# Kernel tuning notes

Measured on AMD Instinct MI355X. Metric: run time of the kernel, lower is better.

## Reference

```python
import jax, jax.numpy as jnp
import numpy as np

N, T, LH, HEADS, C, E = 100000, 24, 64, 4, 16, 1600000
NEG_SLOPE = 0.2  # PyG GATConv leaky_relu slope


def setup_inputs() -> dict:
    key = jax.random.key(0)
    ks = jax.random.split(key, 24)
    s = 0.05
    inp = {
        'input_tensor': jax.random.normal(ks[0], (N, T), jnp.float32),
        'edge_index': jax.random.randint(ks[1], (2, E), 0, N, jnp.int32),
        'edge_attr': jax.random.uniform(ks[2], (E, 1), jnp.float32),
        'knn_mask_short': jax.random.randint(ks[3], (E,), 0, 2, jnp.int32).astype(bool),
        # LSTM layer 1 (input_size=1): gate order i,f,g,o
        'W_ih1': jax.random.normal(ks[4], (4 * LH, 1), jnp.float32) * s,
        'W_hh1': jax.random.normal(ks[5], (4 * LH, LH), jnp.float32) * s,
        'b_ih1': jax.random.normal(ks[6], (4 * LH,), jnp.float32) * s,
        'b_hh1': jax.random.normal(ks[7], (4 * LH,), jnp.float32) * s,
        # LSTM layer 2 (input_size=LH)
        'W_ih2': jax.random.normal(ks[8], (4 * LH, LH), jnp.float32) * s,
        'W_hh2': jax.random.normal(ks[9], (4 * LH, LH), jnp.float32) * s,
        'b_ih2': jax.random.normal(ks[10], (4 * LH,), jnp.float32) * s,
        'b_hh2': jax.random.normal(ks[11], (4 * LH,), jnp.float32) * s,
        # GATConv params
        'gat_lin_w': jax.random.normal(ks[12], (HEADS * C, LH), jnp.float32) * s,
        'gat_lin_edge_w': jax.random.normal(ks[13], (HEADS * C, 1), jnp.float32) * s,
        'att_src': jax.random.normal(ks[14], (HEADS, C), jnp.float32) * s,
        'att_dst': jax.random.normal(ks[15], (HEADS, C), jnp.float32) * s,
        'att_edge': jax.random.normal(ks[16], (HEADS, C), jnp.float32) * s,
        'gat_bias': jax.random.normal(ks[17], (HEADS * C,), jnp.float32) * s,
        # final Linear
        'fc_w': jax.random.normal(ks[18], (1, HEADS * C), jnp.float32) * s,
        'fc_b': jax.random.normal(ks[19], (1,), jnp.float32) * s,
    }
    return inp


def _lstm_cell(x, h, c, W_ih, W_hh, b):
    z = x @ W_ih.T + h @ W_hh.T + b  # (N, 4H)
    i, f, g, o = jnp.split(z, 4, axis=-1)
    c = jax.nn.sigmoid(f) * c + jax.nn.sigmoid(i) * jnp.tanh(g)
    h = jax.nn.sigmoid(o) * jnp.tanh(c)
    return h, c


def reference(input_tensor, edge_index, edge_attr, knn_mask_short,
              W_ih1, W_hh1, b_ih1, b_hh1, W_ih2, W_hh2, b_ih2, b_hh2,
              gat_lin_w, gat_lin_edge_w, att_src, att_dst, att_edge, gat_bias,
              fc_w, fc_b):
    n = input_tensor.shape[0]
    # --- 2-layer LSTM over time, fused per-step (only final h2 needed) ---
    xs = input_tensor.T[:, :, None]  # (T, N, 1)
    b1 = b_ih1 + b_hh1
    b2 = b_ih2 + b_hh2
    z = jnp.zeros((n, LH), input_tensor.dtype)

    def step(carry, x_t):
        h1, c1, h2, c2 = carry
        h1, c1 = _lstm_cell(x_t, h1, c1, W_ih1, W_hh1, b1)
        h2, c2 = _lstm_cell(h1, h2, c2, W_ih2, W_hh2, b2)
        return (h1, c1, h2, c2), None

    (h1, c1, h2, c2), _ = jax.lax.scan(step, (z, z, z, z), xs)
    lstm_out = h2  # (N, LH): last time-step output of layer 2

    # --- GATConv (heads concat, edge_dim=1), eval mode (dropout off) ---
    x = (lstm_out @ gat_lin_w.T).reshape(n, HEADS, C)  # (N, H, C)
    a_src = jnp.einsum('nhc,hc->nh', x, att_src)
    a_dst = jnp.einsum('nhc,hc->nh', x, att_dst)
    src, dst = edge_index[0], edge_index[1]
    e = (edge_attr @ gat_lin_edge_w.T).reshape(-1, HEADS, C)  # (E, H, C)
    a_edge = jnp.einsum('ehc,hc->eh', e, att_edge)
    alpha = jax.nn.leaky_relu(a_src[src] + a_dst[dst] + a_edge, NEG_SLOPE)  # (E, H)
    # mask out non-'short' edges (equivalent to slicing them away)
    alpha = jnp.where(knn_mask_short[:, None], alpha, -1e30)
    amax = jax.ops.segment_max(alpha, dst, num_segments=n)  # (N, H)
    ex = jnp.exp(alpha - amax[dst]) * knn_mask_short[:, None].astype(alpha.dtype)
    denom = jax.ops.segment_sum(ex, dst, num_segments=n)  # (N, H)
    w = ex / jnp.maximum(denom[dst], 1e-16)  # (E, H) attention weights
    msg = x[src] * w[:, :, None]  # (E, H, C)
    out = jax.ops.segment_sum(msg, dst, num_segments=n).reshape(n, HEADS * C) + gat_bias

    out = jax.nn.elu(out)
    y = out @ fc_w.T + fc_b  # (N, 1)
    return y.reshape(n)
```

## Files before the change

### kernel.cpp

```cpp
#include <hip/hip_runtime.h>
#include <hip/hip_bf16.h>

#define T_STEPS 24
#define NSLOPE 0.2f
#define PITCH2 136
#define LOG2E 1.4426950408889634f

typedef _Float16 half8 __attribute__((ext_vector_type(8)));
typedef _Float16 half2_t __attribute__((ext_vector_type(2)));
typedef float floatx4 __attribute__((ext_vector_type(4)));

#if __has_builtin(__builtin_amdgcn_exp2f)
#define EXP2(x) __builtin_amdgcn_exp2f(x)
#else
#define EXP2(x) exp2f(x)
#endif
#define RCP(x) __builtin_amdgcn_rcpf(x)

#define ACT(A0,A1,A2,A3,CS,HP) {                                        \
    float u_ = EXP2(-(A0));                                             \
    float fw = EXP2(-(A1));                                             \
    float v_ = EXP2(-(A2));                                             \
    float xo = EXP2(-(A3));                                             \
    float f_ = RCP(1.f + fw);                                           \
    float ig = (1.f - v_) * RCP((1.f + u_) * (1.f + v_));               \
    float cs = fmaf(f_, (CS), ig * (2.f*LOG2E));                        \
    (CS) = cs;                                                          \
    float z_ = EXP2(-cs);                                               \
    (HP) = (_Float16)((1.f - z_) * RCP((1.f + xo) * (1.f + z_)));       \
}

#define MFMA16(A,B,C) __builtin_amdgcn_mfma_f32_16x16x32_f16((A),(B),(C),0,0,0)

__global__ __launch_bounds__(256) void prep_kernel(
    const float* __restrict__ W_ih1, const float* __restrict__ W_hh1,
    const float* __restrict__ b_ih1, const float* __restrict__ b_hh1,
    const float* __restrict__ W_ih2, const float* __restrict__ W_hh2,
    const float* __restrict__ b_ih2, const float* __restrict__ b_hh2,
    const float* __restrict__ glw, const float* __restrict__ glew,
    const float* __restrict__ atte, const unsigned char* __restrict__ mask_bytes,
    _Float16* __restrict__ W1F, _Float16* __restrict__ W2F, _Float16* __restrict__ W3F,
    float* __restrict__ b2P, float* __restrict__ ke, int* __restrict__ flag,
    int* __restrict__ deg, int nn)
{
    int tid = blockIdx.x*blockDim.x + threadIdx.x;
    int nth = gridDim.x*blockDim.x;
    for (int i = tid; i < nn; i += nth) deg[i] = 0;
    for (int idx = tid; idx < 24576; idx += nth){
        int b = idx & 7;
        int lane = (idx >> 3) & 63;
        int t2 = idx >> 9;
        int kt = t2 % 3;
        int t3 = t2 / 3;
        int m = t3 & 1, w = t3 >> 1;
        int row16 = lane & 15;
        int g = row16 & 3, cl = row16 >> 2;
        int row = g*64 + 8*w + 2*cl + m;
        float sc = (g == 2) ? 2.f*LOG2E : LOG2E;
        int k = (lane>>4)*8 + b;
        float val;
        if (kt < 2){ val = W_hh1[row*64 + 32*kt + k]; }
        else { val = (k == 0) ? W_ih1[row] : (k == 1) ? (b_ih1[row]+b_hh1[row]) : 0.f; }
        W1F[idx] = (_Float16)(val * sc);
    }
    for (int idx = tid; idx < 32768; idx += nth){
        int b = idx & 7;
        int lane = (idx >> 3) & 63;
        int kt = (idx >> 9) & 3;
        int t3 = idx >> 11;
        int m = t3 & 1, w = t3 >> 1;
        int row16 = lane & 15;
        int g = row16 & 3, cl = row16 >> 2;
        int row = g*64 + 8*w + 2*cl + m;
        float sc = (g == 2) ? 2.f*LOG2E : LOG2E;
        int k = 32*kt + (lane>>4)*8 + b;
        W2F[idx] = (_Float16)(((k < 64) ? W_ih2[row*64 + k] : W_hh2[row*64 + (k-64)]) * sc);
    }
    for (int idx = tid; idx < 4096; idx += nth){
        int b = idx & 7, t1 = idx >> 3; int lane = t1 & 63, t2 = t1 >> 6;
        int kt = t2 & 1, w = t2 >> 1;
        int row = 16*w + (lane & 15);
        W3F[idx] = (_Float16)glw[row*64 + 32*kt + (lane>>4)*8 + b];
    }
    for (int idx = tid; idx < 4096; idx += nth){
        int r = idx & 3;
        int lane = (idx >> 2) & 63;
        int m = (idx >> 8) & 1;
        int w = idx >> 9;
        int grp = lane >> 4;
        int row = r*64 + 8*w + 2*grp + m;
        float sc = (r == 2) ? 2.f*LOG2E : LOG2E;
        b2P[idx] = (b_ih2[row] + b_hh2[row]) * sc;
    }
    if (tid < 4){ float s = 0.f; for (int c = 0; c < 16; c++) s += atte[tid*16+c]*glew[tid*16+c]; ke[tid] = s; }
    if (tid == 0){ int nz = 0;
        for (int i = 0; i < 4096; i++){ if ((i&3) != 0 && mask_bytes[i] != 0) nz++; }
        *flag = (nz == 0) ? 1 : 0; }
}

__global__ __launch_bounds__(256) void count_kernel(
    const int* __restrict__ ei, const void* __restrict__ maskp, const int* __restrict__ flag,
    int* __restrict__ deg, int E)
{
    int e = blockIdx.x*256 + threadIdx.x;
    if (e >= E) return;
    bool m = (*flag) ? (((const int*)maskp)[e] != 0) : (((const unsigned char*)maskp)[e] != 0);
    if (!m) return;
    atomicAdd(deg + ei[E + e], 1);
}

__global__ __launch_bounds__(1024) void scan_kernel(
    const int* __restrict__ deg, int* __restrict__ offs, int* __restrict__ cursor, int nn)
{
    __shared__ int wsum[16];
    __shared__ int sbase;
    int lane = threadIdx.x & 63, wv = threadIdx.x >> 6;
    if (threadIdx.x == 0) sbase = 0;
    __syncthreads();
    for (int base = 0; base < nn; base += 4096){
        int i0 = base + (int)threadIdx.x*4;
        int4 v = make_int4(0,0,0,0);
        if (i0 + 3 < nn) v = *(const int4*)(deg + i0);
        else {
            if (i0   < nn) v.x = deg[i0];
            if (i0+1 < nn) v.y = deg[i0+1];
            if (i0+2 < nn) v.z = deg[i0+2];
            if (i0+3 < nn) v.w = deg[i0+3];
        }
        int s = v.x + v.y + v.z + v.w;
        int sc = s;
        #pragma unroll
        for (int o = 1; o < 64; o <<= 1){ int t = __shfl_up(sc, o); if (lane >= o) sc += t; }
        if (lane == 63) wsum[wv] = sc;
        __syncthreads();
        int wbase = 0, total = 0;
        #pragma unroll
        for (int k = 0; k < 16; k++){ int sk = wsum[k]; if (k < wv) wbase += sk; total += sk; }
        int excl = sbase + wbase + sc - s;
        if (i0 < nn){
            int e0 = excl, e1 = e0 + v.x, e2 = e1 + v.y, e3 = e2 + v.z;
            if (i0 + 3 < nn){
                *(int4*)(offs + i0)   = make_int4(e0,e1,e2,e3);
                *(int4*)(cursor + i0) = make_int4(e0,e1,e2,e3);
            } else {
                offs[i0] = e0; cursor[i0] = e0;
                if (i0+1 < nn){ offs[i0+1] = e1; cursor[i0+1] = e1; }
                if (i0+2 < nn){ offs[i0+2] = e2; cursor[i0+2] = e2; }
            }
        }
        __syncthreads();
        if (threadIdx.x == 0) sbase += total;
        __syncthreads();
    }
    if (threadIdx.x == 0) offs[nn] = sbase;
}

__global__ __launch_bounds__(256) void scatter_kernel(
    const int* __restrict__ ei, const float* __restrict__ ea, const void* __restrict__ maskp,
    const int* __restrict__ flag, int* __restrict__ cursor, int2* __restrict__ rec, int E)
{
    int e = blockIdx.x*256 + threadIdx.x;
    if (e >= E) return;
    bool m = (*flag) ? (((const int*)maskp)[e] != 0) : (((const unsigned char*)maskp)[e] != 0);
    if (!m) return;
    int d = ei[E + e];
    int pos = atomicAdd(cursor + d, 1);
    rec[pos] = make_int2(ei[e], __float_as_int(ea[e]));
}

__device__ __forceinline__ void lstm_step(
    const _Float16* RB, _Float16* WB, const _Float16* x_lds, int t,
    const half8 (&w1f)[2][3], const half8 (&w2f)[2][4], const floatx4 (&b2v)[2],
    float* c1s, float* c2s, int col, int grp, int wv)
{
    #pragma unroll
    for (int nt = 0; nt < 2; nt++){
        int node = nt*16 + col;
        half8 bf0 = *(const half8*)&RB[node*PITCH2 + grp*8];
        half8 bf1 = *(const half8*)&RB[node*PITCH2 + 32 + grp*8];
        half8 xb;
        #pragma unroll
        for (int b = 0; b < 8; b++) xb[b] = (_Float16)0.f;
        _Float16 xv = x_lds[node*26 + t];
        if (grp == 0){ xb[0] = xv; xb[1] = (_Float16)1.0f; }
        floatx4 aA = {0,0,0,0}, aB = {0,0,0,0};
        aA = MFMA16(w1f[0][0], bf0, aA);  aB = MFMA16(w1f[1][0], bf0, aB);
        aA = MFMA16(w1f[0][1], bf1, aA);  aB = MFMA16(w1f[1][1], bf1, aB);
        aA = MFMA16(w1f[0][2], xb,  aA);  aB = MFMA16(w1f[1][2], xb,  aB);
        _Float16 hA, hB;
        ACT(aA[0], aA[1], aA[2], aA[3], c1s[nt*2+0], hA);
        ACT(aB[0], aB[1], aB[2], aB[3], c1s[nt*2+1], hB);
        half2_t hh; hh[0] = hA; hh[1] = hB;
        *(half2_t*)&WB[node*PITCH2 + 8*wv + 2*grp] = hh;
    }
    __syncthreads();
    #pragma unroll
    for (int nt = 0; nt < 2; nt++){
        int node = nt*16 + col;
        half8 bf0 = *(const half8*)&WB[node*PITCH2 + grp*8];
        half8 bf1 = *(const half8*)&WB[node*PITCH2 + 32 + grp*8];
        half8 bf2 = *(const half8*)&RB[node*PITCH2 + 64 + grp*8];
        half8 bf3 = *(const half8*)&RB[node*PITCH2 + 96 + grp*8];
        floatx4 aA = b2v[0], aB = b2v[1];
        aA = MFMA16(w2f[0][0], bf0, aA);  aB = MFMA16(w2f[1][0], bf0, aB);
        aA = MFMA16(w2f[0][1], bf1, aA);  aB = MFMA16(w2f[1][1], bf1, aB);
        aA = MFMA16(w2f[0][2], bf2, aA);  aB = MFMA16(w2f[1][2], bf2, aB);
        aA = MFMA16(w2f[0][3], bf3, aA);  aB = MFMA16(w2f[1][3], bf3, aB);
        _Float16 hA, hB;
        ACT(aA[0], aA[1], aA[2], aA[3], c2s[nt*2+0], hA);
        ACT(aB[0], aB[1], aB[2], aB[3], c2s[nt*2+1], hB);
        half2_t hh; hh[0] = hA; hh[1] = hB;
        *(half2_t*)&WB[node*PITCH2 + 64 + 8*wv + 2*grp] = hh;
    }
    __syncthreads();
}

__global__ __launch_bounds__(512) void lstm_kernel(
    const float* __restrict__ x_in,
    const _Float16* __restrict__ W1F, const _Float16* __restrict__ W2F, const _Float16* __restrict__ W3F,
    const float* __restrict__ b2P,
    const float* __restrict__ atts, const float* __restrict__ attd,
    float* __restrict__ x_out, float* __restrict__ a_src, float* __restrict__ a_dst, int nn)
{
    __shared__ _Float16 hbuf0[32*PITCH2];
    __shared__ _Float16 hbuf1[32*PITCH2];
    __shared__ _Float16 x_lds[32*26];

    const int wv   = threadIdx.x >> 6;
    const int lane = threadIdx.x & 63;
    const int grp  = lane >> 4;
    const int col  = lane & 15;
    const int node0 = blockIdx.x * 32;

    for (int i = threadIdx.x; i < 32*T_STEPS; i += 512){
        int node = i / T_STEPS, t = i % T_STEPS;
        int nd = node0 + node;
        x_lds[node*26 + t] = (_Float16)((nd < nn) ? x_in[nd*T_STEPS + t] : 0.f);
    }
    for (int i = threadIdx.x; i < 32*PITCH2/2; i += 512) ((float*)hbuf0)[i] = 0.f;

    const half8* W1Fv = (const half8*)W1F;
    const half8* W2Fv = (const half8*)W2F;
    half8 w1f[2][3], w2f[2][4];
    floatx4 b2v[2];
    #pragma unroll
    for (int m = 0; m < 2; m++){
        #pragma unroll
        for (int kt = 0; kt < 3; kt++) w1f[m][kt] = W1Fv[((wv*2+m)*3+kt)*64 + lane];
        #pragma unroll
        for (int kt = 0; kt < 4; kt++) w2f[m][kt] = W2Fv[((wv*2+m)*4+kt)*64 + lane];
        b2v[m] = *(const floatx4*)&b2P[((wv*2+m)*64 + lane)*4];
    }

    float c1s[4], c2s[4];
    #pragma unroll
    for (int i = 0; i < 4; i++){ c1s[i] = 0.f; c2s[i] = 0.f; }

    __syncthreads();

    for (int t = 0; t < T_STEPS; t += 2){
        lstm_step(hbuf0, hbuf1, x_lds, t,   w1f, w2f, b2v, c1s, c2s, col, grp, wv);
        lstm_step(hbuf1, hbuf0, x_lds, t+1, w1f, w2f, b2v, c1s, c2s, col, grp, wv);
    }

    if (wv < 4){
        const half8* W3Fv = (const half8*)W3F;
        half8 w3f0 = W3Fv[(wv*2+0)*64 + lane];
        half8 w3f1 = W3Fv[(wv*2+1)*64 + lane];
        float asw[4], adw[4];
        #pragma unroll
        for (int r = 0; r < 4; r++){ int ch = 16*wv + grp*4 + r; asw[r] = atts[ch]; adw[r] = attd[ch]; }
        #pragma unroll
        for (int nt = 0; nt < 2; nt++){
            int node = nt*16 + col;
            int nd = node0 + node;
            floatx4 pa = {0,0,0,0};
            half8 bf0 = *(const half8*)&hbuf0[node*PITCH2 + 64 + grp*8];
            half8 bf1 = *(const half8*)&hbuf0[node*PITCH2 + 96 + grp*8];
            pa = MFMA16(w3f0, bf0, pa);
            pa = MFMA16(w3f1, bf1, pa);
            float s  = pa[0]*asw[0] + pa[1]*asw[1] + pa[2]*asw[2] + pa[3]*asw[3];
            float dv = pa[0]*adw[0] + pa[1]*adw[1] + pa[2]*adw[2] + pa[3]*adw[3];
            s  += __shfl_xor(s, 16);  s  += __shfl_xor(s, 32);
            dv += __shfl_xor(dv, 16); dv += __shfl_xor(dv, 32);
            if (nd < nn){
                *(float4*)(x_out + (size_t)nd*64 + 16*wv + grp*4) = make_float4(pa[0], pa[1], pa[2], pa[3]);
                if (grp == 0) a_src[nd*4 + wv] = s;
                else if (grp == 1) a_dst[nd*4 + wv] = dv;
            }
        }
    }
}

__global__ __launch_bounds__(256) void gather_kernel(
    const int2* __restrict__ rec, const int* __restrict__ offs,
    const float* __restrict__ a_src, const float* __restrict__ a_dst, const float* __restrict__ ke,
    const float* __restrict__ xf, const float* __restrict__ gbias,
    const float* __restrict__ fcw, const float* __restrict__ fcb,
    float* __restrict__ y, int nn)
{
    int wv = threadIdx.x >> 6, lane = threadIdx.x & 63;
    int node = blockIdx.x*4 + wv;
    if (node >= nn) return;
    int h = lane >> 4;
    float keh = ke[h];
    float adv = a_dst[4*node + h];
    int beg = offs[node], end = offs[node+1];
    float acc = 0.f, dacc = 0.f;
    int j = beg;
    for (; j + 3 < end; j += 4){
        int2 r0 = rec[j], r1 = rec[j+1], r2 = rec[j+2], r3 = rec[j+3];
        int s0 = r0.x, s1 = r1.x, s2 = r2.x, s3 = r3.x;
        float as0 = a_src[4*s0 + h], as1 = a_src[4*s1 + h];
        float as2 = a_src[4*s2 + h], as3 = a_src[4*s3 + h];
        float x0 = xf[(size_t)s0*64 + lane], x1 = xf[(size_t)s1*64 + lane];
        float x2 = xf[(size_t)s2*64 + lane], x3 = xf[(size_t)s3*64 + lane];
        float a0 = as0 + adv + __int_as_float(r0.y)*keh;
        float a1 = as1 + adv + __int_as_float(r1.y)*keh;
        float a2 = as2 + adv + __int_as_float(r2.y)*keh;
        float a3 = as3 + adv + __int_as_float(r3.y)*keh;
        a0 = a0 > 0.f ? a0 : NSLOPE*a0;
        a1 = a1 > 0.f ? a1 : NSLOPE*a1;
        a2 = a2 > 0.f ? a2 : NSLOPE*a2;
        a3 = a3 > 0.f ? a3 : NSLOPE*a3;
        float e0 = __expf(a0), e1 = __expf(a1), e2 = __expf(a2), e3 = __expf(a3);
        dacc += (e0 + e1) + (e2 + e3);
        acc = fmaf(e0, x0, acc);
        acc = fmaf(e1, x1, acc);
        acc = fmaf(e2, x2, acc);
        acc = fmaf(e3, x3, acc);
    }
    for (; j < end; ++j){
        int2 r = rec[j];
        int s = r.x;
        float a = a_src[4*s + h] + adv + __int_as_float(r.y)*keh;
        a = a > 0.f ? a : NSLOPE*a;
        float ev = __expf(a);
        dacc += ev;
        acc = fmaf(ev, xf[(size_t)s*64 + lane], acc);
    }
    float v = acc * RCP(fmaxf(dacc, 1e-16f)) + gbias[lane];
    v = v > 0.f ? v : (__expf(v) - 1.f);
    float r2 = v * fcw[lane];
    #pragma unroll
    for (int off = 1; off < 64; off <<= 1) r2 += __shfl_xor(r2, off, 64);
    if (lane == 0) y[node] = r2 + fcb[0];
}

extern "C" void kernel_launch(void* const* d_in, const int* in_sizes, int n_in,
                              void* d_out, int out_size, void* d_ws, size_t ws_size,
                              hipStream_t stream)
{
    const float* x_in  = (const float*)d_in[0];
    const int*   ei    = (const int*)d_in[1];
    const float* ea    = (const float*)d_in[2];
    const void*  mask  = d_in[3];
    const float* W_ih1 = (const float*)d_in[4];
    const float* W_hh1 = (const float*)d_in[5];
    const float* b_ih1 = (const float*)d_in[6];
    const float* b_hh1 = (const float*)d_in[7];
    const float* W_ih2 = (const float*)d_in[8];
    const float* W_hh2 = (const float*)d_in[9];
    const float* b_ih2 = (const float*)d_in[10];
    const float* b_hh2 = (const float*)d_in[11];
    const float* glw   = (const float*)d_in[12];
    const float* glew  = (const float*)d_in[13];
    const float* atts  = (const float*)d_in[14];
    const float* attd  = (const float*)d_in[15];
    const float* atte  = (const float*)d_in[16];
    const float* gbias = (const float*)d_in[17];
    const float* fcw   = (const float*)d_in[18];
    const float* fcb   = (const float*)d_in[19];

    const int NN = in_sizes[0] / T_STEPS;
    const int E  = in_sizes[1] / 2;

    float* ws = (float*)d_ws;
    size_t o = 0;
    _Float16* W1F = (_Float16*)(ws + o); o += 24576/2;
    _Float16* W2F = (_Float16*)(ws + o); o += 32768/2;
    _Float16* W3F = (_Float16*)(ws + o); o += 4096/2;
    float* b2P = ws + o; o += 4096;
    float* ke  = ws + o; o += 64;
    int*  flag = (int*)(ws + o); o += 64;
    float* asrc= ws + o; o += (size_t)NN*4;
    float* adst= ws + o; o += (size_t)NN*4;
    float* xf  = ws + o; o += (size_t)NN*64;
    int* deg    = (int*)(ws + o); o += NN;
    int* offs   = (int*)(ws + o); o += NN + 64;
    int* cursor = (int*)(ws + o); o += NN;
    int2* rec   = (int2*)(ws + o); o += (size_t)E*2;

    prep_kernel<<<128, 256, 0, stream>>>(W_ih1, W_hh1, b_ih1, b_hh1, W_ih2, W_hh2, b_ih2, b_hh2,
                                         glw, glew, atte, (const unsigned char*)mask,
                                         W1F, W2F, W3F, b2P, ke, flag, deg, NN);
    count_kernel<<<(E + 255)/256, 256, 0, stream>>>(ei, mask, flag, deg, E);
    scan_kernel<<<1, 1024, 0, stream>>>(deg, offs, cursor, NN);
    scatter_kernel<<<(E + 255)/256, 256, 0, stream>>>(ei, ea, mask, flag, cursor, rec, E);
    lstm_kernel<<<(NN + 31)/32, 512, 0, stream>>>(x_in, W1F, W2F, W3F, b2P,
                                                  atts, attd, xf, asrc, adst, NN);
    gather_kernel<<<(NN + 3)/4, 256, 0, stream>>>(rec, offs, asrc, adst, ke, xf,
                                                  gbias, fcw, fcb, (float*)d_out, NN);
}
```

Measured before the change: 605.4 us.

## Fuse edge degree counting into LSTM kernel via interleaved block roles

Merges the count kernel into the LSTM kernel as a horizontal fusion: blocks are interleaved between LSTM tiles and edge-degree counting so that the memory/atomic-bound counting overlaps with the compute-bound LSTM. Scan and scatter now run after the LSTM finishes rather than before. This removes one launch and hides the counting cost. In exchange, count blocks reserve the large LDS footprint of the LSTM kernel, which can limit occupancy for them.

```diff
diff --git a/kernel.cpp b/kernel.cpp
--- a/kernel.cpp
+++ b/kernel.cpp
@@ -98,17 +98,6 @@
         *flag = (nz == 0) ? 1 : 0; }
 }
 
-__global__ __launch_bounds__(256) void count_kernel(
-    const int* __restrict__ ei, const void* __restrict__ maskp, const int* __restrict__ flag,
-    int* __restrict__ deg, int E)
-{
-    int e = blockIdx.x*256 + threadIdx.x;
-    if (e >= E) return;
-    bool m = (*flag) ? (((const int*)maskp)[e] != 0) : (((const unsigned char*)maskp)[e] != 0);
-    if (!m) return;
-    atomicAdd(deg + ei[E + e], 1);
-}
-
 __global__ __launch_bounds__(1024) void scan_kernel(
     const int* __restrict__ deg, int* __restrict__ offs, int* __restrict__ cursor, int nn)
 {
@@ -215,22 +204,40 @@
     __syncthreads();
 }
 
-__global__ __launch_bounds__(512) void lstm_kernel(
+__global__ __launch_bounds__(512) void lstm_count_kernel(
     const float* __restrict__ x_in,
     const _Float16* __restrict__ W1F, const _Float16* __restrict__ W2F, const _Float16* __restrict__ W3F,
     const float* __restrict__ b2P,
     const float* __restrict__ atts, const float* __restrict__ attd,
-    float* __restrict__ x_out, float* __restrict__ a_src, float* __restrict__ a_dst, int nn)
+    float* __restrict__ x_out, float* __restrict__ a_src, float* __restrict__ a_dst, int nn,
+    const int* __restrict__ ei, const void* __restrict__ maskp, const int* __restrict__ flag,
+    int* __restrict__ deg, int E, int LB, int CB)
 {
     __shared__ _Float16 hbuf0[32*PITCH2];
     __shared__ _Float16 hbuf1[32*PITCH2];
     __shared__ _Float16 x_lds[32*26];
+
+    int b = blockIdx.x;
+    int nmin = (LB < CB) ? LB : CB;
+    int sub;
+    bool is_lstm;
+    if (b < 2*nmin){ is_lstm = ((b & 1) == 0); sub = b >> 1; }
+    else { sub = nmin + (b - 2*nmin); is_lstm = (LB > CB); }
+
+    if (!is_lstm){
+        int e = sub*512 + (int)threadIdx.x;
+        if (e < E){
+            bool m = (*flag) ? (((const int*)maskp)[e] != 0) : (((const unsigned char*)maskp)[e] != 0);
+            if (m) atomicAdd(deg + ei[E + e], 1);
+        }
+        return;
+    }
 
     const int wv   = threadIdx.x >> 6;
     const int lane = threadIdx.x & 63;
     const int grp  = lane >> 4;
     const int col  = lane & 15;
-    const int node0 = blockIdx.x * 32;
+    const int node0 = sub * 32;
 
     for (int i = threadIdx.x; i < 32*T_STEPS; i += 512){
         int node = i / T_STEPS, t = i % T_STEPS;
@@ -391,14 +398,17 @@
     int* cursor = (int*)(ws + o); o += NN;
     int2* rec   = (int2*)(ws + o); o += (size_t)E*2;
 
+    const int LB = (NN + 31)/32;
+    const int CB = (E + 511)/512;
+
     prep_kernel<<<128, 256, 0, stream>>>(W_ih1, W_hh1, b_ih1, b_hh1, W_ih2, W_hh2, b_ih2, b_hh2,
                                          glw, glew, atte, (const unsigned char*)mask,
                                          W1F, W2F, W3F, b2P, ke, flag, deg, NN);
-    count_kernel<<<(E + 255)/256, 256, 0, stream>>>(ei, mask, flag, deg, E);
+    lstm_count_kernel<<<LB + CB, 512, 0, stream>>>(x_in, W1F, W2F, W3F, b2P,
+                                                   atts, attd, xf, asrc, adst, NN,
+                                                   ei, mask, flag, deg, E, LB, CB);
     scan_kernel<<<1, 1024, 0, stream>>>(deg, offs, cursor, NN);
     scatter_kernel<<<(E + 255)/256, 256, 0, stream>>>(ei, ea, mask, flag, cursor, rec, E);
-    lstm_kernel<<<(NN + 31)/32, 512, 0, stream>>>(x_in, W1F, W2F, W3F, b2P,
-                                                  atts, attd, xf, asrc, adst, NN);
     gather_kernel<<<(NN + 3)/4, 256, 0, stream>>>(rec, offs, asrc, adst, ke, xf,
                                                   gbias, fcw, fcb, (float*)d_out, NN);
 }
```

Result: slower. 919.2 us (+51.8%).
